# Kernel optimization log

Measured on AMD Instinct MI355X. Metric: run time of the kernel, lower is better.

## Reference

```python
import jax, jax.numpy as jnp
import numpy as np

H = 16
N_TASKS, N_DATA, N_DEV = 400_000, 200_000, 8


def _edges(key, n_src, n_dst, e):
    k1, k2 = jax.random.split(key)
    src = jax.random.randint(k1, (e,), 0, n_src)
    dst = jax.random.randint(k2, (e,), 0, n_dst)
    return jnp.stack([src, dst]).astype(jnp.int64)


def setup_inputs() -> dict:
    key = jax.random.key(0)
    ks = jax.random.split(key, 16)
    inp = {
        "x_tasks": jax.random.normal(ks[0], (N_TASKS, 12), jnp.float32),
        "x_data": jax.random.normal(ks[1], (N_DATA, 5), jnp.float32),
        "x_devices": jax.random.normal(ks[2], (N_DEV, 12), jnp.float32),
        "ei_data_tasks": _edges(ks[3], N_DATA, N_TASKS, 1_600_000),
        "ei_tasks_data": _edges(ks[4], N_TASKS, N_DATA, 1_600_000),
        "ei_tasks_devices": _edges(ks[5], N_TASKS, N_DEV, 400_000),
        "ei_devices_tasks": _edges(ks[6], N_DEV, N_TASKS, 400_000),
        "ei_data_devices": _edges(ks[7], N_DATA, N_DEV, 200_000),
        "ei_devices_data": _edges(ks[8], N_DEV, N_DATA, 200_000),
        "ei_tt_to": _edges(ks[9], N_TASKS, N_TASKS, 800_000),
        "ei_tt_from": _edges(ks[10], N_TASKS, N_TASKS, 800_000),
        # stacked GraphConv weights, grouped by input dim
        # W_rel5:  [0]=data->tasks, [1]=data->devices
        "W_rel5": jax.random.normal(ks[11], (2, 5, H), jnp.float32) * 0.3,
        # W_rel12: [0]=tasks->data,[1]=tasks->devices,[2]=devices->tasks,[3]=devices->data,[4]=tt_to,[5]=tt_from
        "W_rel12": jax.random.normal(ks[12], (6, 12, H), jnp.float32) * 0.2,
        # b_rel order: dt_t, t_d, t_dev, dev_t, d_dev, dev_d, tt_to, tt_from
        "b_rel": jax.random.normal(ks[13], (8, H), jnp.float32) * 0.1,
        # W_root5: [0]=tasks->data (dst data), [1]=devices->data
        "W_root5": jax.random.normal(ks[14], (2, 5, H), jnp.float32) * 0.3,
        # W_root12: [0]=data->tasks,[1]=tasks->devices,[2]=devices->tasks,[3]=data->devices,[4]=tt_to,[5]=tt_from
        "W_root12": jax.random.normal(ks[15], (6, 12, H), jnp.float32) * 0.2,
        # LayerNorm params: [0]=tasks, [1]=data, [2]=devices
        "ln_gamma": jnp.ones((3, H), jnp.float32),
        "ln_beta": jnp.zeros((3, H), jnp.float32),
    }
    return inp


def _graph_conv(x_src, x_dst, ei, W_rel, b_rel, W_root):
    # PyG GraphConv(aggr='add'): lin_rel(scatter_add(x_src[src] -> dst)) + lin_root(x_dst)
    agg = jax.ops.segment_sum(x_src[ei[0]], ei[1], num_segments=x_dst.shape[0])
    return agg @ W_rel + b_rel + x_dst @ W_root


def _layer_norm(x, gamma, beta, eps=1e-5):
    mu = jnp.mean(x, axis=-1, keepdims=True)
    var = jnp.mean(jnp.square(x - mu), axis=-1, keepdims=True)
    return (x - mu) * jax.lax.rsqrt(var + eps) * gamma + beta


def reference(x_tasks, x_data, x_devices,
              ei_data_tasks, ei_tasks_data, ei_tasks_devices, ei_devices_tasks,
              ei_data_devices, ei_devices_data, ei_tt_to, ei_tt_from,
              W_rel5, W_rel12, b_rel, W_root5, W_root12, ln_gamma, ln_beta):
    # HeteroConv(aggr='sum'): sum relation outputs per destination node type
    tasks = (
        _graph_conv(x_data, x_tasks, ei_data_tasks, W_rel5[0], b_rel[0], W_root12[0])
        + _graph_conv(x_devices, x_tasks, ei_devices_tasks, W_rel12[2], b_rel[3], W_root12[2])
        + _graph_conv(x_tasks, x_tasks, ei_tt_to, W_rel12[4], b_rel[6], W_root12[4])
        + _graph_conv(x_tasks, x_tasks, ei_tt_from, W_rel12[5], b_rel[7], W_root12[5])
    )
    data = (
        _graph_conv(x_tasks, x_data, ei_tasks_data, W_rel12[0], b_rel[1], W_root5[0])
        + _graph_conv(x_devices, x_data, ei_devices_data, W_rel12[3], b_rel[5], W_root5[1])
    )
    devices = (
        _graph_conv(x_tasks, x_devices, ei_tasks_devices, W_rel12[1], b_rel[2], W_root12[1])
        + _graph_conv(x_data, x_devices, ei_data_devices, W_rel5[1], b_rel[4], W_root12[3])
    )
    slope = 0.01
    tasks = jax.nn.leaky_relu(_layer_norm(tasks, ln_gamma[0], ln_beta[0]), slope)
    data = jax.nn.leaky_relu(_layer_norm(data, ln_gamma[1], ln_beta[1]), slope)
    devices = jax.nn.leaky_relu(_layer_norm(devices, ln_gamma[2], ln_beta[2]), slope)
    return tasks, data, devices
```

## Files before the change

kernel.cpp:

```cpp
#include <hip/hip_runtime.h>
#include <hip/hip_fp16.h>

#define LRELU(v) ((v) >= 0.0f ? (v) : 0.01f * (v))
#define EPB 8192
#define SHIFT 7
#define PAIRS 1600

struct PartDesc {
    const int* src; const int* dst;
    unsigned* part; int* cursor;
    int E, B, cap, chunk0;
    unsigned tag;
};

struct PrepArgs {
    PartDesc r[6];
    int part_end;
    const int *tdev_e; int E_tdev; int sd12_b0, sd12_nb;
    const int *ddev_e; int E_ddev; int sd5_b0, sd5_nb;
    const float *x_tasks, *x_data, *x_dev;
    float *aggT_dev, *aggD_dev;
    __half *h_tasks; int NT; int ct_b0;
    __half *h_data;  int ND; int cd_b0;
};

template<int F>
__device__ __forceinline__ void loadrow(const float* __restrict__ x, unsigned s, float* v) {
    const float* p = x + (size_t)s * F;
    #pragma unroll
    for (int f = 0; f < F; ++f) v[f] = p[f];
}
template<>
__device__ __forceinline__ void loadrow<12>(const float* __restrict__ x, unsigned s, float* v) {
    const float4* p = (const float4*)(x + (size_t)s * 12);
    float4 a = p[0], b = p[1], c = p[2];
    v[0]=a.x; v[1]=a.y; v[2]=a.z; v[3]=a.w;
    v[4]=b.x; v[5]=b.y; v[6]=b.z; v[7]=b.w;
    v[8]=c.x; v[9]=c.y; v[10]=c.z; v[11]=c.w;
}

template<int F>
__device__ void scatter_dev_body(const float* __restrict__ x, const int* __restrict__ src,
                                 const int* __restrict__ dst, int E,
                                 float* __restrict__ agg, float* s_agg,
                                 int bl, int nb, int t)
{
    for (int i = t; i < 8 * F; i += 256) s_agg[i] = 0.0f;
    __syncthreads();
    const int stride = nb * 256;
    for (int e = bl * 256 + t; e < E; e += stride) {
        float v[F];
        loadrow<F>(x, (unsigned)src[e], v);
        int d = dst[e];
        #pragma unroll
        for (int f = 0; f < F; ++f) atomicAdd(&s_agg[d * F + f], v[f]);
    }
    __syncthreads();
    if (t < 8 * F) atomicAdd(&agg[t], s_agg[t]);
}

__global__ __launch_bounds__(256)
void prep_k(PrepArgs A)
{
    __shared__ unsigned shp[2 * PAIRS];
    const int bid = blockIdx.x;
    const int t = threadIdx.x;

    if (bid < A.part_end) {
        unsigned* hist = shp;
        unsigned* base = shp + PAIRS;
        int ri = 0;
        #pragma unroll
        for (int k = 1; k < 6; ++k) if (bid >= A.r[k].chunk0) ri = k;
        const PartDesc d = A.r[ri];
        const int e0 = (bid - d.chunk0) * EPB;
        const int e1 = min(d.E, e0 + EPB);
        const int npair = (d.B + 1) >> 1;

        for (int i = t; i < npair; i += 256) hist[i] = 0u;
        __syncthreads();
        for (int e = e0 + t; e < e1; e += 256) {
            int b = d.dst[e] >> SHIFT;
            atomicAdd(&hist[b >> 1], 1u << ((b & 1) << 4));
        }
        __syncthreads();
        for (int i = t; i < npair; i += 256) {
            unsigned h = hist[i];
            unsigned lo = h & 0xffffu, hi = h >> 16;
            unsigned blo = lo ? (unsigned)atomicAdd(&d.cursor[2 * i],     (int)lo) : 0u;
            unsigned bhi = hi ? (unsigned)atomicAdd(&d.cursor[2 * i + 1], (int)hi) : 0u;
            base[i] = (blo & 0xffffu) | (bhi << 16);
            hist[i] = 0u;
        }
        __syncthreads();
        for (int e = e0 + t; e < e1; e += 256) {
            int dd = d.dst[e];
            int b = dd >> SHIFT;
            unsigned s16 = (unsigned)(b & 1) << 4;
            unsigned r = atomicAdd(&hist[b >> 1], 1u << s16);
            unsigned idx = ((r >> s16) & 0xffffu) + ((base[b >> 1] >> s16) & 0xffffu);
            if ((int)idx < d.cap)
                d.part[(size_t)b * d.cap + idx] =
                    ((unsigned)d.src[e] << 9) | (((unsigned)dd & 127u) << 2) | d.tag;
        }
    } else if (bid < A.sd5_b0) {
        scatter_dev_body<12>(A.x_tasks, A.tdev_e, A.tdev_e + A.E_tdev, A.E_tdev,
                             A.aggT_dev, (float*)shp, bid - A.sd12_b0, A.sd12_nb, t);
    } else if (bid < A.ct_b0) {
        scatter_dev_body<5>(A.x_data, A.ddev_e, A.ddev_e + A.E_ddev, A.E_ddev,
                            A.aggD_dev, (float*)shp, bid - A.sd5_b0, A.sd5_nb, t);
    } else if (bid < A.cd_b0) {
        int row = (bid - A.ct_b0) * 256 + t;
        if (row < A.NT) {
            const float* xr = A.x_tasks + (size_t)row * 12;
            __half h[16];
            #pragma unroll
            for (int j = 0; j < 12; ++j) h[j] = __float2half(xr[j]);
            #pragma unroll
            for (int j = 12; j < 16; ++j) h[j] = __half(0.0f);
            uint4* dst = (uint4*)(A.h_tasks + (size_t)row * 16);
            dst[0] = *(const uint4*)h;
            dst[1] = *(const uint4*)(h + 8);
        }
    } else {
        int row = (bid - A.cd_b0) * 256 + t;
        if (row < A.ND) {
            const float* xr = A.x_data + (size_t)row * 5;
            __half h[8];
            #pragma unroll
            for (int j = 0; j < 5; ++j) h[j] = __float2half(xr[j]);
            #pragma unroll
            for (int j = 5; j < 8; ++j) h[j] = __half(0.0f);
            *(uint4*)(A.h_data + (size_t)row * 8) = *(const uint4*)h;
        }
    }
}

struct FusedArgs {
    const unsigned *p_task, *p_data;
    const int *c_task, *c_data;
    int cap_t, cap_d;
    const __half *h_tasks, *h_data;
    const float *x_dev, *x_tasks, *x_data;
    const float *aggT_dev, *aggD_dev;
    const float *W_rel5, *W_rel12, *b_rel, *W_root5, *W_root12, *ln_g, *ln_b;
    float *out_tasks, *out_data, *out_dev;
    int NT, ND, NDEV, Bt, Bd;
};

__device__ __forceinline__ void issue_task(unsigned e, const FusedArgs& A, uint4* r) {
    unsigned rel = e & 3u, s = e >> 9;
    if (rel == 0u) {
        r[0] = *(const uint4*)(A.h_data + (size_t)s * 8);
    } else if (rel == 1u) {
        const uint4* q = (const uint4*)(A.x_dev + (size_t)s * 12);
        r[0] = q[0]; r[1] = q[1]; r[2] = q[2];
    } else {
        const uint4* q = (const uint4*)(A.h_tasks + (size_t)s * 16);
        r[0] = q[0]; r[1] = q[1];
    }
}
__device__ __forceinline__ void commit_task(unsigned e, const uint4* r, float* acc) {
    unsigned rel = e & 3u;
    float* a = acc + ((e >> 2) & 127u) * 41;
    if (rel == 0u) {
        const __half2* h = (const __half2*)r;
        float2 f0 = __half22float2(h[0]), f1 = __half22float2(h[1]), f2 = __half22float2(h[2]);
        atomicAdd(a + 0, f0.x); atomicAdd(a + 1, f0.y);
        atomicAdd(a + 2, f1.x); atomicAdd(a + 3, f1.y);
        atomicAdd(a + 4, f2.x);
    } else if (rel == 1u) {
        const float* f = (const float*)r;
        #pragma unroll
        for (int j = 0; j < 12; ++j) atomicAdd(a + 5 + j, f[j]);
    } else {
        float* base = a + (rel == 2u ? 17 : 29);
        const __half2* h = (const __half2*)r;
        #pragma unroll
        for (int j = 0; j < 6; ++j) {
            float2 f = __half22float2(h[j]);
            atomicAdd(base + 2 * j,     f.x);
            atomicAdd(base + 2 * j + 1, f.y);
        }
    }
}

__device__ __forceinline__ void issue_data(unsigned e, const FusedArgs& A, uint4* r) {
    unsigned rel = e & 3u, s = e >> 9;
    if (rel == 0u) {
        const uint4* q = (const uint4*)(A.h_tasks + (size_t)s * 16);
        r[0] = q[0]; r[1] = q[1];
    } else {
        const uint4* q = (const uint4*)(A.x_dev + (size_t)s * 12);
        r[0] = q[0]; r[1] = q[1]; r[2] = q[2];
    }
}
__device__ __forceinline__ void commit_data(unsigned e, const uint4* r, float* acc) {
    unsigned rel = e & 3u;
    float* a = acc + ((e >> 2) & 127u) * 25;
    if (rel == 0u) {
        const __half2* h = (const __half2*)r;
        #pragma unroll
        for (int j = 0; j < 6; ++j) {
            float2 f = __half22float2(h[j]);
            atomicAdd(a + 2 * j,     f.x);
            atomicAdd(a + 2 * j + 1, f.y);
        }
    } else {
        const float* f = (const float*)r;
        #pragma unroll
        for (int j = 0; j < 12; ++j) atomicAdd(a + 12 + j, f[j]);
    }
}

__device__ __forceinline__
void ln_store(float* o, const float* __restrict__ sg, const float* __restrict__ sbt,
              float* __restrict__ op)
{
    float mu = 0.0f;
    #pragma unroll
    for (int k = 0; k < 16; ++k) mu += o[k];
    mu *= 0.0625f;
    float var = 0.0f;
    #pragma unroll
    for (int k = 0; k < 16; ++k) { float d = o[k] - mu; var = fmaf(d, d, var); }
    var *= 0.0625f;
    const float r = rsqrtf(var + 1e-5f);
    #pragma unroll
    for (int k = 0; k < 16; ++k) {
        float v = (o[k] - mu) * r * sg[k] + sbt[k];
        o[k] = LRELU(v);
    }
    float4* q = (float4*)op;
    const float4* s = (const float4*)o;
    q[0] = s[0]; q[1] = s[1]; q[2] = s[2]; q[3] = s[3];
}

__global__ __launch_bounds__(512, 8)
void fused_k(FusedArgs A)
{
    __shared__ __align__(16) float lds[6144];
    const int bid = blockIdx.x;
    const int t = threadIdx.x;

    if (bid < A.Bt) {
        float* acc = lds;
        float* sW  = lds + 5248;
        float* sb  = lds + 6096;
        float* sg  = lds + 6112;
        float* sbt = lds + 6128;

        for (int i = t; i < 5248; i += 512) acc[i] = 0.0f;
        for (int i = t; i < 80; i += 512) sW[i] = A.W_rel5[i];
        for (int i = t; i < 192; i += 512) {
            sW[80  + i] = A.W_rel12[384 + i];
            sW[272 + i] = A.W_rel12[768 + i];
            sW[464 + i] = A.W_rel12[960 + i];
            sW[656 + i] = A.W_root12[i] + A.W_root12[384 + i]
                        + A.W_root12[768 + i] + A.W_root12[960 + i];
        }
        if (t < 16) {
            sb[t]  = A.b_rel[t] + A.b_rel[48 + t] + A.b_rel[96 + t] + A.b_rel[112 + t];
            sg[t]  = A.ln_g[t];
            sbt[t] = A.ln_b[t];
        }
        __syncthreads();

        const unsigned* p = A.p_task + (size_t)bid * A.cap_t;
        const int cnt = min(A.c_task[bid], A.cap_t);
        int i = t;
        for (; i + 512 < cnt; i += 1024) {
            unsigned e0 = p[i], e1 = p[i + 512];
            uint4 r0[3], r1[3];
            issue_task(e0, A, r0);
            issue_task(e1, A, r1);
            commit_task(e0, r0, acc);
            commit_task(e1, r1, acc);
        }
        if (i < cnt) {
            unsigned e = p[i];
            uint4 r[3];
            issue_task(e, A, r);
            commit_task(e, r, acc);
        }
        __syncthreads();

        const int node = t >> 2, part = t & 3;
        const int row = (bid << SHIFT) + node;
        if (row < A.NT) {
            const float* ar = acc + node * 41;
            const int p4 = part * 4;
            float o0 = sb[p4], o1 = sb[p4 + 1], o2 = sb[p4 + 2], o3 = sb[p4 + 3];
            #pragma unroll
            for (int f = 0; f < 41; ++f) {
                float v = ar[f];
                float4 w = *(const float4*)(sW + f * 16 + p4);
                o0 = fmaf(v, w.x, o0); o1 = fmaf(v, w.y, o1);
                o2 = fmaf(v, w.z, o2); o3 = fmaf(v, w.w, o3);
            }
            const float* xr = A.x_tasks + (size_t)row * 12;
            #pragma unroll
            for (int f = 0; f < 12; ++f) {
                float v = xr[f];
                float4 w = *(const float4*)(sW + (41 + f) * 16 + p4);
                o0 = fmaf(v, w.x, o0); o1 = fmaf(v, w.y, o1);
                o2 = fmaf(v, w.z, o2); o3 = fmaf(v, w.w, o3);
            }
            float s = o0 + o1 + o2 + o3;
            s += __shfl_xor(s, 1); s += __shfl_xor(s, 2);
            const float mu = s * 0.0625f;
            float d0 = o0 - mu, d1 = o1 - mu, d2 = o2 - mu, d3 = o3 - mu;
            float q = d0*d0 + d1*d1 + d2*d2 + d3*d3;
            q += __shfl_xor(q, 1); q += __shfl_xor(q, 2);
            const float r = rsqrtf(q * 0.0625f + 1e-5f);
            float4 out;
            out.x = LRELU(d0 * r * sg[p4]     + sbt[p4]);
            out.y = LRELU(d1 * r * sg[p4 + 1] + sbt[p4 + 1]);
            out.z = LRELU(d2 * r * sg[p4 + 2] + sbt[p4 + 2]);
            out.w = LRELU(d3 * r * sg[p4 + 3] + sbt[p4 + 3]);
            *(float4*)(A.out_tasks + (size_t)row * 16 + p4) = out;
        }
    } else if (bid < A.Bt + A.Bd) {
        float* acc = lds;
        float* sW  = lds + 3200;
        float* sb  = lds + 3664;
        float* sg  = lds + 3680;
        float* sbt = lds + 3696;

        for (int i = t; i < 3200; i += 512) acc[i] = 0.0f;
        for (int i = t; i < 192; i += 512) {
            sW[i]       = A.W_rel12[i];
            sW[192 + i] = A.W_rel12[576 + i];
        }
        for (int i = t; i < 80; i += 512)
            sW[384 + i] = A.W_root5[i] + A.W_root5[80 + i];
        if (t < 16) {
            sb[t]  = A.b_rel[16 + t] + A.b_rel[80 + t];
            sg[t]  = A.ln_g[16 + t];
            sbt[t] = A.ln_b[16 + t];
        }
        __syncthreads();

        const int b = bid - A.Bt;
        const unsigned* p = A.p_data + (size_t)b * A.cap_d;
        const int cnt = min(A.c_data[b], A.cap_d);
        int i = t;
        for (; i + 512 < cnt; i += 1024) {
            unsigned e0 = p[i], e1 = p[i + 512];
            uint4 r0[3], r1[3];
            issue_data(e0, A, r0);
            issue_data(e1, A, r1);
            commit_data(e0, r0, acc);
            commit_data(e1, r1, acc);
        }
        if (i < cnt) {
            unsigned e = p[i];
            uint4 r[3];
            issue_data(e, A, r);
            commit_data(e, r, acc);
        }
        __syncthreads();

        const int node = t >> 2, part = t & 3;
        const int row = (b << SHIFT) + node;
        if (row < A.ND) {
            const float* ar = acc + node * 25;
            const int p4 = part * 4;
            float o0 = sb[p4], o1 = sb[p4 + 1], o2 = sb[p4 + 2], o3 = sb[p4 + 3];
            #pragma unroll
            for (int f = 0; f < 24; ++f) {
                float v = ar[f];
                float4 w = *(const float4*)(sW + f * 16 + p4);
                o0 = fmaf(v, w.x, o0); o1 = fmaf(v, w.y, o1);
                o2 = fmaf(v, w.z, o2); o3 = fmaf(v, w.w, o3);
            }
            const float* xr = A.x_data + (size_t)row * 5;
            #pragma unroll
            for (int f = 0; f < 5; ++f) {
                float v = xr[f];
                float4 w = *(const float4*)(sW + (24 + f) * 16 + p4);
                o0 = fmaf(v, w.x, o0); o1 = fmaf(v, w.y, o1);
                o2 = fmaf(v, w.z, o2); o3 = fmaf(v, w.w, o3);
            }
            float s = o0 + o1 + o2 + o3;
            s += __shfl_xor(s, 1); s += __shfl_xor(s, 2);
            const float mu = s * 0.0625f;
            float d0 = o0 - mu, d1 = o1 - mu, d2 = o2 - mu, d3 = o3 - mu;
            float q = d0*d0 + d1*d1 + d2*d2 + d3*d3;
            q += __shfl_xor(q, 1); q += __shfl_xor(q, 2);
            const float r = rsqrtf(q * 0.0625f + 1e-5f);
            float4 out;
            out.x = LRELU(d0 * r * sg[p4]     + sbt[p4]);
            out.y = LRELU(d1 * r * sg[p4 + 1] + sbt[p4 + 1]);
            out.z = LRELU(d2 * r * sg[p4 + 2] + sbt[p4 + 2]);
            out.w = LRELU(d3 * r * sg[p4 + 3] + sbt[p4 + 3]);
            *(float4*)(A.out_data + (size_t)row * 16 + p4) = out;
        }
    } else {
        const int i = t;
        if (i < A.NDEV) {
            float o[16];
            #pragma unroll
            for (int k = 0; k < 16; ++k) o[k] = A.b_rel[32 + k] + A.b_rel[64 + k];
            #pragma unroll
            for (int j = 0; j < 12; ++j) {
                float fj = A.aggT_dev[i * 12 + j];
                #pragma unroll
                for (int k = 0; k < 16; ++k) o[k] = fmaf(fj, A.W_rel12[192 + j * 16 + k], o[k]);
            }
            #pragma unroll
            for (int j = 0; j < 5; ++j) {
                float fj = A.aggD_dev[i * 5 + j];
                #pragma unroll
                for (int k = 0; k < 16; ++k) o[k] = fmaf(fj, A.W_rel5[80 + j * 16 + k], o[k]);
            }
            #pragma unroll
            for (int j = 0; j < 12; ++j) {
                float fj = A.x_dev[i * 12 + j];
                #pragma unroll
                for (int k = 0; k < 16; ++k)
                    o[k] = fmaf(fj, A.W_root12[192 + j * 16 + k] + A.W_root12[576 + j * 16 + k], o[k]);
            }
            ln_store(o, A.ln_g + 32, A.ln_b + 32, A.out_dev + (size_t)i * 16);
        }
    }
}

extern "C" void kernel_launch(void* const* d_in, const int* in_sizes, int n_in,
                              void* d_out, int out_size, void* d_ws, size_t ws_size,
                              hipStream_t stream)
{
    const float* x_tasks = (const float*)d_in[0];
    const float* x_data  = (const float*)d_in[1];
    const float* x_dev   = (const float*)d_in[2];
    const int* ei_dt    = (const int*)d_in[3];
    const int* ei_td    = (const int*)d_in[4];
    const int* ei_tdev  = (const int*)d_in[5];
    const int* ei_devt  = (const int*)d_in[6];
    const int* ei_ddev  = (const int*)d_in[7];
    const int* ei_devd  = (const int*)d_in[8];
    const int* ei_to    = (const int*)d_in[9];
    const int* ei_from  = (const int*)d_in[10];
    const float* W_rel5   = (const float*)d_in[11];
    const float* W_rel12  = (const float*)d_in[12];
    const float* b_rel    = (const float*)d_in[13];
    const float* W_root5  = (const float*)d_in[14];
    const float* W_root12 = (const float*)d_in[15];
    const float* ln_g     = (const float*)d_in[16];
    const float* ln_b     = (const float*)d_in[17];

    const int NT   = in_sizes[0] / 12;
    const int ND   = in_sizes[1] / 5;
    const int NDEV = in_sizes[2] / 12;
    const int E_dt   = in_sizes[3]  / 2;
    const int E_td   = in_sizes[4]  / 2;
    const int E_tdev = in_sizes[5]  / 2;
    const int E_devt = in_sizes[6]  / 2;
    const int E_ddev = in_sizes[7]  / 2;
    const int E_devd = in_sizes[8]  / 2;
    const int E_to   = in_sizes[9]  / 2;
    const int E_from = in_sizes[10] / 2;

    const int B_t = (NT + 127) / 128;
    const int B_d = (ND + 127) / 128;

    auto capf = [](long long E, int B) {
        int mean = (int)(E / B) + 1;
        int c = mean + mean / 4 + 128;
        return (c + 3) & ~3;
    };
    const int cap_t = capf((long long)E_dt + E_devt + E_to + E_from, B_t);
    const int cap_d = capf((long long)E_td + E_devd, B_d);

    float* ws = (float*)d_ws;
    size_t o = 0;
    int* c_task = (int*)(ws + o); o += 3200;
    int* c_data = (int*)(ws + o); o += 1600;
    float* aggT_dev = ws + o; o += 96;
    float* aggD_dev = ws + o; o += 48;
    const size_t zero_bytes = o * sizeof(float);
    o = (o + 3) & ~(size_t)3;
    __half* h_tasks = (__half*)(ws + o); o += (size_t)NT * 8;
    __half* h_data  = (__half*)(ws + o); o += (size_t)ND * 4;
    unsigned* p_task = (unsigned*)(ws + o); o += (size_t)B_t * cap_t;
    unsigned* p_data = (unsigned*)(ws + o); o += (size_t)B_d * cap_d;

    hipMemsetAsync(d_ws, 0, zero_bytes, stream);

    auto nc = [](int e) { return (e + EPB - 1) / EPB; };
    PrepArgs pa;
    int ch = 0;
    pa.r[0] = { ei_dt,   ei_dt   + E_dt,   p_task, c_task, E_dt,   B_t, cap_t, ch, 0u }; ch += nc(E_dt);
    pa.r[1] = { ei_devt, ei_devt + E_devt, p_task, c_task, E_devt, B_t, cap_t, ch, 1u }; ch += nc(E_devt);
    pa.r[2] = { ei_to,   ei_to   + E_to,   p_task, c_task, E_to,   B_t, cap_t, ch, 2u }; ch += nc(E_to);
    pa.r[3] = { ei_from, ei_from + E_from, p_task, c_task, E_from, B_t, cap_t, ch, 3u }; ch += nc(E_from);
    pa.r[4] = { ei_td,   ei_td   + E_td,   p_data, c_data, E_td,   B_d, cap_d, ch, 0u }; ch += nc(E_td);
    pa.r[5] = { ei_devd, ei_devd + E_devd, p_data, c_data, E_devd, B_d, cap_d, ch, 1u }; ch += nc(E_devd);
    pa.part_end = ch;
    pa.tdev_e = ei_tdev; pa.E_tdev = E_tdev; pa.sd12_b0 = ch; pa.sd12_nb = 192; ch += 192;
    pa.ddev_e = ei_ddev; pa.E_ddev = E_ddev; pa.sd5_b0  = ch; pa.sd5_nb  = 96;  ch += 96;
    pa.x_tasks = x_tasks; pa.x_data = x_data; pa.x_dev = x_dev;
    pa.aggT_dev = aggT_dev; pa.aggD_dev = aggD_dev;
    pa.h_tasks = h_tasks; pa.NT = NT; pa.ct_b0 = ch; ch += (NT + 255) / 256;
    pa.h_data  = h_data;  pa.ND = ND; pa.cd_b0 = ch; ch += (ND + 255) / 256;

    prep_k<<<ch, 256, 0, stream>>>(pa);

    float* out_tasks = (float*)d_out;
    float* out_data  = out_tasks + (size_t)NT * 16;
    float* out_dev   = out_data  + (size_t)ND * 16;

    FusedArgs fa;
    fa.p_task = p_task; fa.p_data = p_data;
    fa.c_task = c_task; fa.c_data = c_data;
    fa.cap_t = cap_t; fa.cap_d = cap_d;
    fa.h_tasks = h_tasks; fa.h_data = h_data;
    fa.x_dev = x_dev; fa.x_tasks = x_tasks; fa.x_data = x_data;
    fa.aggT_dev = aggT_dev; fa.aggD_dev = aggD_dev;
    fa.W_rel5 = W_rel5; fa.W_rel12 = W_rel12; fa.b_rel = b_rel;
    fa.W_root5 = W_root5; fa.W_root12 = W_root12; fa.ln_g = ln_g; fa.ln_b = ln_b;
    fa.out_tasks = out_tasks; fa.out_data = out_data; fa.out_dev = out_dev;
    fa.NT = NT; fa.ND = ND; fa.NDEV = NDEV;
    fa.Bt = B_t; fa.Bd = B_d;

    fused_k<<<B_t + B_d + 1, 512, 0, stream>>>(fa);
}
```

Before: 597.9 us.

## Triple-issue edge gathers, nontemporal loads/stores, retune EPB, occupancy and bucket capacity

The edge-gather loop in the fused task and data blocks now issues three edges per thread up front, covering typical bucket sizes in one batch, before committing to LDS. Edge indices, task features and outputs move through nontemporal loads and stores. The x_tasks row is loaded early as vector loads, and the x_data pointer setup is hoisted. Edges per partition block rise, launch-bounds occupancy drops from 8 to 6, and bucket capacity slack shrinks, which risks overflow truncation on skewed buckets.

```diff
diff --git a/kernel.cpp b/kernel.cpp
--- a/kernel.cpp
+++ b/kernel.cpp
@@ -2,9 +2,11 @@
 #include <hip/hip_fp16.h>
 
 #define LRELU(v) ((v) >= 0.0f ? (v) : 0.01f * (v))
-#define EPB 8192
+#define EPB 32768
 #define SHIFT 7
 #define PAIRS 1600
+
+typedef float nfloat4 __attribute__((ext_vector_type(4)));
 
 struct PartDesc {
     const int* src; const int* dst;
@@ -236,7 +238,7 @@
     q[0] = s[0]; q[1] = s[1]; q[2] = s[2]; q[3] = s[3];
 }
 
-__global__ __launch_bounds__(512, 8)
+__global__ __launch_bounds__(512, 6)
 void fused_k(FusedArgs A)
 {
     __shared__ __align__(16) float lds[6144];
@@ -268,20 +270,25 @@
 
         const unsigned* p = A.p_task + (size_t)bid * A.cap_t;
         const int cnt = min(A.c_task[bid], A.cap_t);
-        int i = t;
-        for (; i + 512 < cnt; i += 1024) {
-            unsigned e0 = p[i], e1 = p[i + 512];
-            uint4 r0[3], r1[3];
-            issue_task(e0, A, r0);
-            issue_task(e1, A, r1);
-            commit_task(e0, r0, acc);
-            commit_task(e1, r1, acc);
-        }
-        if (i < cnt) {
-            unsigned e = p[i];
-            uint4 r[3];
-            issue_task(e, A, r);
-            commit_task(e, r, acc);
+        {
+            const bool v0 = t < cnt, v1 = t + 512 < cnt, v2 = t + 1024 < cnt;
+            unsigned e0 = 0, e1 = 0, e2 = 0;
+            uint4 r0[3], r1[3], r2[3];
+            if (v0) e0 = __builtin_nontemporal_load(p + t);
+            if (v1) e1 = __builtin_nontemporal_load(p + t + 512);
+            if (v2) e2 = __builtin_nontemporal_load(p + t + 1024);
+            if (v0) issue_task(e0, A, r0);
+            if (v1) issue_task(e1, A, r1);
+            if (v2) issue_task(e2, A, r2);
+            if (v0) commit_task(e0, r0, acc);
+            if (v1) commit_task(e1, r1, acc);
+            if (v2) commit_task(e2, r2, acc);
+            for (int i = t + 1536; i < cnt; i += 512) {
+                unsigned e = p[i];
+                uint4 r[3];
+                issue_task(e, A, r);
+                commit_task(e, r, acc);
+            }
         }
         __syncthreads();
 
@@ -290,6 +297,10 @@
         if (row < A.NT) {
             const float* ar = acc + node * 41;
             const int p4 = part * 4;
+            const nfloat4* xr = (const nfloat4*)(A.x_tasks + (size_t)row * 12);
+            nfloat4 x0 = __builtin_nontemporal_load(xr);
+            nfloat4 x1 = __builtin_nontemporal_load(xr + 1);
+            nfloat4 x2 = __builtin_nontemporal_load(xr + 2);
             float o0 = sb[p4], o1 = sb[p4 + 1], o2 = sb[p4 + 2], o3 = sb[p4 + 3];
             #pragma unroll
             for (int f = 0; f < 41; ++f) {
@@ -298,10 +309,10 @@
                 o0 = fmaf(v, w.x, o0); o1 = fmaf(v, w.y, o1);
                 o2 = fmaf(v, w.z, o2); o3 = fmaf(v, w.w, o3);
             }
-            const float* xr = A.x_tasks + (size_t)row * 12;
+            float xf[12] = {x0.x,x0.y,x0.z,x0.w, x1.x,x1.y,x1.z,x1.w, x2.x,x2.y,x2.z,x2.w};
             #pragma unroll
             for (int f = 0; f < 12; ++f) {
-                float v = xr[f];
+                float v = xf[f];
                 float4 w = *(const float4*)(sW + (41 + f) * 16 + p4);
                 o0 = fmaf(v, w.x, o0); o1 = fmaf(v, w.y, o1);
                 o2 = fmaf(v, w.z, o2); o3 = fmaf(v, w.w, o3);
@@ -313,12 +324,12 @@
             float q = d0*d0 + d1*d1 + d2*d2 + d3*d3;
             q += __shfl_xor(q, 1); q += __shfl_xor(q, 2);
             const float r = rsqrtf(q * 0.0625f + 1e-5f);
-            float4 out;
+            nfloat4 out;
             out.x = LRELU(d0 * r * sg[p4]     + sbt[p4]);
             out.y = LRELU(d1 * r * sg[p4 + 1] + sbt[p4 + 1]);
             out.z = LRELU(d2 * r * sg[p4 + 2] + sbt[p4 + 2]);
             out.w = LRELU(d3 * r * sg[p4 + 3] + sbt[p4 + 3]);
-            *(float4*)(A.out_tasks + (size_t)row * 16 + p4) = out;
+            __builtin_nontemporal_store(out, (nfloat4*)(A.out_tasks + (size_t)row * 16 + p4));
         }
     } else if (bid < A.Bt + A.Bd) {
         float* acc = lds;
@@ -344,20 +355,25 @@
         const int b = bid - A.Bt;
         const unsigned* p = A.p_data + (size_t)b * A.cap_d;
         const int cnt = min(A.c_data[b], A.cap_d);
-        int i = t;
-        for (; i + 512 < cnt; i += 1024) {
-            unsigned e0 = p[i], e1 = p[i + 512];
-            uint4 r0[3], r1[3];
-            issue_data(e0, A, r0);
-            issue_data(e1, A, r1);
-            commit_data(e0, r0, acc);
-            commit_data(e1, r1, acc);
-        }
-        if (i < cnt) {
-            unsigned e = p[i];
-            uint4 r[3];
-            issue_data(e, A, r);
-            commit_data(e, r, acc);
+        {
+            const bool v0 = t < cnt, v1 = t + 512 < cnt, v2 = t + 1024 < cnt;
+            unsigned e0 = 0, e1 = 0, e2 = 0;
+            uint4 r0[3], r1[3], r2[3];
+            if (v0) e0 = __builtin_nontemporal_load(p + t);
+            if (v1) e1 = __builtin_nontemporal_load(p + t + 512);
+            if (v2) e2 = __builtin_nontemporal_load(p + t + 1024);
+            if (v0) issue_data(e0, A, r0);
+            if (v1) issue_data(e1, A, r1);
+            if (v2) issue_data(e2, A, r2);
+            if (v0) commit_data(e0, r0, acc);
+            if (v1) commit_data(e1, r1, acc);
+            if (v2) commit_data(e2, r2, acc);
+            for (int i = t + 1536; i < cnt; i += 512) {
+                unsigned e = p[i];
+                uint4 r[3];
+                issue_data(e, A, r);
+                commit_data(e, r, acc);
+            }
         }
         __syncthreads();
 
@@ -366,6 +382,7 @@
         if (row < A.ND) {
             const float* ar = acc + node * 25;
             const int p4 = part * 4;
+            const float* xr = A.x_data + (size_t)row * 5;
             float o0 = sb[p4], o1 = sb[p4 + 1], o2 = sb[p4 + 2], o3 = sb[p4 + 3];
             #pragma unroll
             for (int f = 0; f < 24; ++f) {
@@ -374,7 +391,6 @@
                 o0 = fmaf(v, w.x, o0); o1 = fmaf(v, w.y, o1);
                 o2 = fmaf(v, w.z, o2); o3 = fmaf(v, w.w, o3);
             }
-            const float* xr = A.x_data + (size_t)row * 5;
             #pragma unroll
             for (int f = 0; f < 5; ++f) {
                 float v = xr[f];
@@ -389,12 +405,12 @@
             float q = d0*d0 + d1*d1 + d2*d2 + d3*d3;
             q += __shfl_xor(q, 1); q += __shfl_xor(q, 2);
             const float r = rsqrtf(q * 0.0625f + 1e-5f);
-            float4 out;
+            nfloat4 out;
             out.x = LRELU(d0 * r * sg[p4]     + sbt[p4]);
             out.y = LRELU(d1 * r * sg[p4 + 1] + sbt[p4 + 1]);
             out.z = LRELU(d2 * r * sg[p4 + 2] + sbt[p4 + 2]);
             out.w = LRELU(d3 * r * sg[p4 + 3] + sbt[p4 + 3]);
-            *(float4*)(A.out_data + (size_t)row * 16 + p4) = out;
+            __builtin_nontemporal_store(out, (nfloat4*)(A.out_data + (size_t)row * 16 + p4));
         }
     } else {
         const int i = t;
@@ -466,7 +482,7 @@
 
     auto capf = [](long long E, int B) {
         int mean = (int)(E / B) + 1;
-        int c = mean + mean / 4 + 128;
+        int c = mean + mean / 8 + 128;
         return (c + 3) & ~3;
     };
     const int cap_t = capf((long long)E_dt + E_devt + E_to + E_from, B_t);
```

Measured after the change: 660.3 us. 10.4% more time.
